# Kernel tuning notes

Measured on AMD Instinct MI355X. Metric: run time of the kernel, lower is better.

The kernel has to match this reference:

```python
import jax, jax.numpy as jnp
import numpy as np

NUM_HEADS = 16
ROPE_THETA = 10000.0


def apply_rope(x, pos):
    # x: [b, h, s, d_head]; rotates consecutive pairs (2i, 2i+1)
    d = x.shape[-1]
    inv_freq = ROPE_THETA ** (-jnp.arange(0, d, 2, dtype=x.dtype) / d)  # [d/2]
    ang = pos.astype(x.dtype)[:, None] * inv_freq[None, :]              # [s, d/2]
    cos, sin = jnp.cos(ang), jnp.sin(ang)
    x1, x2 = x[..., 0::2], x[..., 1::2]
    rot = jnp.stack([x1 * cos - x2 * sin, x1 * sin + x2 * cos], axis=-1)
    return rot.reshape(x.shape)


def setup_inputs() -> dict:
    key = jax.random.key(0)
    k1, k2, k3 = jax.random.split(key, 3)
    d_model = 1024
    x = jax.random.normal(k1, (4, 2048, d_model), dtype=jnp.float32)
    wqkv = jax.random.normal(k2, (3 * d_model, d_model), dtype=jnp.float32) * 0.02
    wout = jax.random.normal(k3, (d_model, d_model), dtype=jnp.float32) * 0.02
    return {"x": x, "wqkv": wqkv, "wout": wout}


def reference(x, wqkv, wout):
    b, s, d_model = x.shape
    h = NUM_HEADS
    d_head = d_model // h

    qkv = jnp.einsum("bsd,ed->bse", x, wqkv)              # [b, s, 3*d_model]
    q, k, v = jnp.split(qkv, 3, axis=-1)

    def split_heads(t):  # [b, s, d_model] -> [b, h, s, d_head]
        return t.reshape(b, s, h, d_head).transpose(0, 2, 1, 3)

    q, k, v = split_heads(q), split_heads(k), split_heads(v)

    pos = jnp.arange(s)
    q = apply_rope(q, pos)
    k = apply_rope(k, pos)

    scale = 1.0 / jnp.sqrt(jnp.asarray(d_head, dtype=x.dtype))
    scores = jnp.einsum("bhqd,bhkd->bhqk", q, k) * scale   # [b, h, s, s]
    causal = jnp.tril(jnp.ones((s, s), dtype=bool))
    scores = jnp.where(causal, scores, jnp.finfo(scores.dtype).min)
    attn = jax.nn.softmax(scores, axis=-1)
    y = jnp.einsum("bhqk,bhkd->bhqd", attn, v)             # [b, h, s, d_head]
    y = y.transpose(0, 2, 1, 3).reshape(b, s, d_model)
    return jnp.einsum("bsd,ed->bse", y, wout)
```

## Files before the change

### kernel.cpp

```cpp
#include <hip/hip_runtime.h>
#include <stdint.h>

typedef uint16_t u16;
typedef __bf16 bf16x8 __attribute__((ext_vector_type(8)));
typedef float   f32x4 __attribute__((ext_vector_type(4)));
typedef uint16_t u16x2 __attribute__((ext_vector_type(2)));
typedef uint16_t u16x4 __attribute__((ext_vector_type(4)));
typedef uint16_t u16x8 __attribute__((ext_vector_type(8)));
typedef float   f32x4g __attribute__((ext_vector_type(4)));

#define DEV __device__ __forceinline__

DEV u16 f2bf(float f) {
  __bf16 h = (__bf16)f;
  return __builtin_bit_cast(u16, h);
}
DEV float bf2f(u16 u) {
  union { uint32_t u; float f; } v; v.u = ((uint32_t)u) << 16;
  return v.f;
}
DEV float exp2fast(float x) {
  float r; asm("v_exp_f32 %0, %1" : "=v"(r) : "v"(x)); return r;
}

DEV void gload_lds16(const u16* g, u16* l) {
  __builtin_amdgcn_global_load_lds((const __attribute__((address_space(1))) void*)g,
                                   (__attribute__((address_space(3))) void*)l,
                                   16, 0, 0);
}

__global__ void sctab_kernel(float2* __restrict__ tab) {
  const int idx = blockIdx.x * 256 + threadIdx.x;
  const int s = idx >> 5, i = idx & 31;
  const float invf = (float)exp2(-2.0 * (double)i / 64.0 * 13.287712379549449);
  float sn, cs;
  sincosf((float)s * invf, &sn, &cs);
  tab[idx] = make_float2(cs, sn);
}

__global__ void cvt3_kernel(const float* __restrict__ a, u16* __restrict__ da,
                            const float* __restrict__ b, u16* __restrict__ db,
                            const float* __restrict__ c, u16* __restrict__ dc) {
  int i = blockIdx.x * 256 + threadIdx.x;
  const float* s; u16* d; int off;
  if (i < 2097152)      { s = a; d = da; off = i; }
  else if (i < 2883584) { s = b; d = db; off = i - 2097152; }
  else                  { s = c; d = dc; off = i - 2883584; }
  f32x4g v = ((const f32x4g*)s)[off];
  u16 tmp[4] = {f2bf(v[0]), f2bf(v[1]), f2bf(v[2]), f2bf(v[3])};
  *(uint64_t*)(d + (size_t)off * 4) = *(const uint64_t*)tmp;
}

__global__ __launch_bounds__(256) void gemm_qkv(const u16* __restrict__ A,
                                                const u16* __restrict__ B,
                                                const float2* __restrict__ tab,
                                                u16* __restrict__ Qh,
                                                u16* __restrict__ Kh,
                                                u16* __restrict__ Vt) {
  constexpr int K = 1024;
  constexpr int BK = 32;
  __shared__ __align__(16) u16 SM[4][128 * BK];
  const int t = threadIdx.x;
  const int w = t >> 6, l = t & 63;
  const int l4 = l >> 4, l15 = l & 15;

  const int nbx = gridDim.x;
  const int nwg = gridDim.x * gridDim.y;
  const int orig = blockIdx.y * nbx + blockIdx.x;
  const int wgid = (orig & 7) * (nwg >> 3) + (orig >> 3);
  const int bm = (wgid / nbx) * 128, bn = (wgid % nbx) * 128;

  const int wr = (w >> 1) * 64, wc = (w & 1) * 64;

  const int srow = w * 32 + (l >> 2);
  const int scol = (l & 3) * 8;
  const u16* gA = A + (size_t)(bm + srow) * K + scol;
  const u16* gB = B + (size_t)(bn + srow) * K + scol;

  f32x4 acc[4][4];
#pragma unroll
  for (int m = 0; m < 4; ++m)
#pragma unroll
    for (int n = 0; n < 4; ++n) acc[m][n] = f32x4{0.f, 0.f, 0.f, 0.f};

  const int nkt = K / BK;

  auto stage = [&](int kt, int buf) {
    const u16* a0 = gA + (size_t)kt * BK;
    const u16* b0 = gB + (size_t)kt * BK;
    gload_lds16(a0,                  &SM[buf][(w * 32) * BK]);
    gload_lds16(a0 + (size_t)16 * K, &SM[buf][(w * 32 + 16) * BK]);
    gload_lds16(b0,                  &SM[2 + buf][(w * 32) * BK]);
    gload_lds16(b0 + (size_t)16 * K, &SM[2 + buf][(w * 32 + 16) * BK]);
  };

  stage(0, 0);
  __syncthreads();
  for (int kt = 0; kt < nkt; ++kt) {
    const int buf = kt & 1;
    if (kt + 1 < nkt) stage(kt + 1, buf ^ 1);
    bf16x8 af[4], bfr[4];
#pragma unroll
    for (int m = 0; m < 4; ++m) af[m]  = *(const bf16x8*)&SM[buf][(wr + m * 16 + l15) * BK + l4 * 8];
#pragma unroll
    for (int n = 0; n < 4; ++n) bfr[n] = *(const bf16x8*)&SM[2 + buf][(wc + n * 16 + l15) * BK + l4 * 8];
#pragma unroll
    for (int m = 0; m < 4; ++m)
#pragma unroll
      for (int n = 0; n < 4; ++n)
        acc[m][n] = __builtin_amdgcn_mfma_f32_16x16x32_bf16(af[m], bfr[n], acc[m][n], 0, 0, 0);
    __syncthreads();
  }

  constexpr int LDW = 132;
  float* Lf = (float*)SM;
  const int part = bn >> 10;
  const int cb = bn & 1023;
  const float qs = (part == 0) ? 0.18033688011112042f : 1.0f;
  u16* const Out = (part == 0) ? Qh : Kh;
  const int lrbase = (w >> 1) * 16 + l4 * 4;
  const int lcbase = (w & 1) * 64 + l15;

#pragma unroll
  for (int m = 0; m < 4; ++m) {
    if (m) __syncthreads();
#pragma unroll
    for (int n = 0; n < 4; ++n)
#pragma unroll
      for (int r = 0; r < 4; ++r)
        Lf[(lrbase + r) * LDW + lcbase + n * 16] = acc[m][n][r];
    __syncthreads();

    if (part != 2) {
      const int rr = t >> 3;
      const int c0 = (t & 7) * 16;
      const int grow = bm + (rr >> 4) * 64 + m * 16 + (rr & 15);
      const int bb = grow >> 11, ss = grow & 2047;
      float f[16];
#pragma unroll
      for (int j = 0; j < 4; ++j)
        *(f32x4g*)&f[j * 4] = *(const f32x4g*)&Lf[rr * LDW + c0 + j * 4];
      const int cc0 = cb + c0;
      const int hh = cc0 >> 6, dd0 = cc0 & 63;
      const float2* tp = &tab[(size_t)ss * 32 + (dd0 >> 1)];
      u16 ob[16];
#pragma unroll
      for (int jp = 0; jp < 8; ++jp) {
        const float2 cs2 = tp[jp];
        ob[2 * jp]     = f2bf((f[2 * jp] * cs2.x - f[2 * jp + 1] * cs2.y) * qs);
        ob[2 * jp + 1] = f2bf((f[2 * jp] * cs2.y + f[2 * jp + 1] * cs2.x) * qs);
      }
      u16* op = Out + ((size_t)(bb * 16 + hh) * 2048 + ss) * 64 + dd0;
      *(u16x8*)op       = *(u16x8*)ob;
      *(u16x8*)(op + 8) = *(u16x8*)(ob + 8);
    } else {
      const int c = t >> 1, half = t & 1;
      const int cc = cb + c, hh = cc >> 6, dd = cc & 63;
      const int g0 = bm + half * 64 + m * 16;
      const int bb = g0 >> 11, ss0 = g0 & 2047;
      u16 ob[16];
#pragma unroll
      for (int j = 0; j < 16; ++j)
        ob[j] = f2bf(Lf[(half * 16 + j) * LDW + c]);
      u16* vp = Vt + ((size_t)(bb * 16 + hh) * 64 + dd) * 2048 + ss0;
      *(u16x8*)vp       = *(u16x8*)ob;
      *(u16x8*)(vp + 8) = *(u16x8*)(ob + 8);
    }
  }
}

template<bool OUT_BF16>
__global__ __launch_bounds__(256) void gemm_bt(const u16* __restrict__ A,
                                               const u16* __restrict__ B,
                                               void* __restrict__ Cv,
                                               int M, int N, int K) {
  constexpr int BK = 32;
  __shared__ __align__(16) u16 As[2][128 * BK];
  __shared__ __align__(16) u16 Bs[2][128 * BK];
  const int t = threadIdx.x;
  const int w = t >> 6, l = t & 63;
  const int l4 = l >> 4, l15 = l & 15;

  const int nbx = gridDim.x;
  const int nwg = gridDim.x * gridDim.y;
  const int orig = blockIdx.y * nbx + blockIdx.x;
  const int wgid = (orig & 7) * (nwg >> 3) + (orig >> 3);
  const int bm = (wgid / nbx) * 128, bn = (wgid % nbx) * 128;

  const int wr = (w >> 1) * 64, wc = (w & 1) * 64;

  const int srow = w * 32 + (l >> 2);
  const int scol = (l & 3) * 8;
  const u16* gA = A + (size_t)(bm + srow) * K + scol;
  const u16* gB = B + (size_t)(bn + srow) * K + scol;

  f32x4 acc[4][4];
#pragma unroll
  for (int m = 0; m < 4; ++m)
#pragma unroll
    for (int n = 0; n < 4; ++n) acc[m][n] = f32x4{0.f, 0.f, 0.f, 0.f};

  const int nkt = K / BK;

  auto stage = [&](int kt, int buf) {
    const u16* a0 = gA + (size_t)kt * BK;
    const u16* b0 = gB + (size_t)kt * BK;
    gload_lds16(a0,                  &As[buf][(w * 32) * BK]);
    gload_lds16(a0 + (size_t)16 * K, &As[buf][(w * 32 + 16) * BK]);
    gload_lds16(b0,                  &Bs[buf][(w * 32) * BK]);
    gload_lds16(b0 + (size_t)16 * K, &Bs[buf][(w * 32 + 16) * BK]);
  };

  stage(0, 0);
  __syncthreads();
  for (int kt = 0; kt < nkt; ++kt) {
    const int buf = kt & 1;
    if (kt + 1 < nkt) stage(kt + 1, buf ^ 1);
    bf16x8 af[4], bfr[4];
#pragma unroll
    for (int m = 0; m < 4; ++m) af[m]  = *(const bf16x8*)&As[buf][(wr + m * 16 + l15) * BK + l4 * 8];
#pragma unroll
    for (int n = 0; n < 4; ++n) bfr[n] = *(const bf16x8*)&Bs[buf][(wc + n * 16 + l15) * BK + l4 * 8];
#pragma unroll
    for (int m = 0; m < 4; ++m)
#pragma unroll
      for (int n = 0; n < 4; ++n)
        acc[m][n] = __builtin_amdgcn_mfma_f32_16x16x32_bf16(af[m], bfr[n], acc[m][n], 0, 0, 0);
    __syncthreads();
  }

#pragma unroll
  for (int m = 0; m < 4; ++m) {
    const int row0 = bm + wr + m * 16 + l4 * 4;
#pragma unroll
    for (int n = 0; n < 4; ++n) {
      const int col = bn + wc + n * 16 + l15;
#pragma unroll
      for (int r = 0; r < 4; ++r) {
        if (OUT_BF16) ((u16*)Cv)[(size_t)(row0 + r) * N + col] = f2bf(acc[m][n][r]);
        else          ((float*)Cv)[(size_t)(row0 + r) * N + col] = acc[m][n][r];
      }
    }
  }
}

__global__ __launch_bounds__(256, 5) void attn_kernel(const u16* __restrict__ Qh,
                                                      const u16* __restrict__ Kh,
                                                      const u16* __restrict__ Vt,
                                                      u16* __restrict__ Y) {
  __shared__ __align__(16) u16 Ks[64][72];
  __shared__ __align__(16) u16 Vs[64][72];
  __shared__ __align__(16) u16 Ps[4][16][72];
  const int t = threadIdx.x, w = t >> 6, l = t & 63;
  const int l4 = l >> 4, l15 = l & 15;
  const int bid = blockIdx.x;
  const int s   = 31 - (bid >> 6);
  const int bh  = bid & 63;
  const int b = bh >> 4, h = bh & 15;
  const int q0 = s * 64 + w * 16;
  const u16* Qb = Qh + (size_t)bh * 2048 * 64;
  const u16* Kb = Kh + (size_t)bh * 2048 * 64;
  const u16* Vb = Vt + (size_t)bh * 64 * 2048;

  bf16x8 qf[2];
#pragma unroll
  for (int ks = 0; ks < 2; ++ks)
    qf[ks] = *(const bf16x8*)(Qb + (size_t)(q0 + l15) * 64 + ks * 32 + l4 * 8);

  f32x4 o[4];
#pragma unroll
  for (int nd = 0; nd < 4; ++nd) o[nd] = f32x4{0.f, 0.f, 0.f, 0.f};
  float lsum = 0.f;

  const int sr = t >> 3;
  const int scol = (t & 7) * 8;
  const int nkv = s + 1;

  u16x8 rk0 = *(const u16x8*)(Kb + (size_t)sr * 64 + scol);
  u16x8 rk1 = *(const u16x8*)(Kb + (size_t)(sr + 32) * 64 + scol);
  u16x8 rv0 = *(const u16x8*)(Vb + (size_t)sr * 2048 + scol);
  u16x8 rv1 = *(const u16x8*)(Vb + (size_t)(sr + 32) * 2048 + scol);

  for (int kv = 0; kv < nkv; ++kv) {
    const int kv0 = kv * 64;
    __syncthreads();
    *(u16x8*)&Ks[sr][scol]      = rk0;
    *(u16x8*)&Ks[sr + 32][scol] = rk1;
    *(u16x8*)&Vs[sr][scol]      = rv0;
    *(u16x8*)&Vs[sr + 32][scol] = rv1;
    __syncthreads();
    if (kv + 1 < nkv) {
      const int n0 = kv0 + 64;
      rk0 = *(const u16x8*)(Kb + (size_t)(n0 + sr) * 64 + scol);
      rk1 = *(const u16x8*)(Kb + (size_t)(n0 + sr + 32) * 64 + scol);
      rv0 = *(const u16x8*)(Vb + (size_t)sr * 2048 + n0 + scol);
      rv1 = *(const u16x8*)(Vb + (size_t)(sr + 32) * 2048 + n0 + scol);
    }

    f32x4 sfr[4];
    __builtin_amdgcn_s_setprio(1);
#pragma unroll
    for (int n = 0; n < 4; ++n) {
      bf16x8 kf0 = *(const bf16x8*)&Ks[n * 16 + l15][l4 * 8];
      bf16x8 kf1 = *(const bf16x8*)&Ks[n * 16 + l15][32 + l4 * 8];
      f32x4 a = f32x4{0.f, 0.f, 0.f, 0.f};
      a = __builtin_amdgcn_mfma_f32_16x16x32_bf16(kf0, qf[0], a, 0, 0, 0);
      a = __builtin_amdgcn_mfma_f32_16x16x32_bf16(kf1, qf[1], a, 0, 0, 0);
      sfr[n] = a;
    }
    __builtin_amdgcn_s_setprio(0);
    if (kv == s) {
      const int q = q0 + l15;
#pragma unroll
      for (int n = 0; n < 4; ++n)
#pragma unroll
        for (int r = 0; r < 4; ++r)
          if (kv0 + n * 16 + l4 * 4 + r > q) sfr[n][r] = -1e30f;
    }
    float rs = 0.f;
#pragma unroll
    for (int n = 0; n < 4; ++n) {
#pragma unroll
      for (int r = 0; r < 4; ++r) {
        const float pv = exp2fast(sfr[n][r]);
        sfr[n][r] = pv; rs += pv;
      }
      u16x4 pk = {f2bf(sfr[n][0]), f2bf(sfr[n][1]), f2bf(sfr[n][2]), f2bf(sfr[n][3])};
      *(u16x4*)&Ps[w][l15][n * 16 + l4 * 4] = pk;
    }
    lsum += rs;

    bf16x8 vfr[4][2];
#pragma unroll
    for (int nd = 0; nd < 4; ++nd) {
      vfr[nd][0] = *(const bf16x8*)&Vs[nd * 16 + l15][l4 * 8];
      vfr[nd][1] = *(const bf16x8*)&Vs[nd * 16 + l15][32 + l4 * 8];
    }
    bf16x8 pf0 = *(const bf16x8*)&Ps[w][l15][l4 * 8];
    bf16x8 pf1 = *(const bf16x8*)&Ps[w][l15][32 + l4 * 8];
    __builtin_amdgcn_s_setprio(1);
#pragma unroll
    for (int nd = 0; nd < 4; ++nd) {
      o[nd] = __builtin_amdgcn_mfma_f32_16x16x32_bf16(pf0, vfr[nd][0], o[nd], 0, 0, 0);
      o[nd] = __builtin_amdgcn_mfma_f32_16x16x32_bf16(pf1, vfr[nd][1], o[nd], 0, 0, 0);
    }
    __builtin_amdgcn_s_setprio(0);
  }

  lsum += __shfl_xor(lsum, 16);
  lsum += __shfl_xor(lsum, 32);
  const float li = 1.0f / lsum;
  float lb[4];
#pragma unroll
  for (int r = 0; r < 4; ++r) lb[r] = __shfl(li, (l & 48) | (l4 * 4 + r));
#pragma unroll
  for (int r = 0; r < 4; ++r) {
    const size_t row = (size_t)b * 2048 + q0 + l4 * 4 + r;
#pragma unroll
    for (int nd = 0; nd < 4; ++nd)
      Y[row * 1024 + h * 64 + nd * 16 + l15] = f2bf(o[nd][r] * lb[r]);
  }
}

extern "C" void kernel_launch(void* const* d_in, const int* in_sizes, int n_in,
                              void* d_out, int out_size, void* d_ws, size_t ws_size,
                              hipStream_t stream) {
  const float* x    = (const float*)d_in[0];
  const float* wqkv = (const float*)d_in[1];
  const float* wout = (const float*)d_in[2];
  float* out = (float*)d_out;
  char* ws = (char*)d_ws;

  u16* x_bf    = (u16*)(ws);
  u16* Y       = x_bf;
  u16* wqkv_bf = (u16*)(ws + 16777216);
  u16* wout_bf = (u16*)(ws + 23068672);
  float2* tab  = (float2*)(ws + 25165824);
  u16* Qh      = (u16*)(ws + 75497472);
  u16* Kh      = (u16*)(ws + 92274688);
  u16* Vt      = (u16*)(ws + 109051904);

  sctab_kernel<<<256, 256, 0, stream>>>(tab);
  cvt3_kernel<<<12288, 256, 0, stream>>>(x, x_bf, wqkv, wqkv_bf, wout, wout_bf);
  gemm_qkv<<<dim3(24, 64), 256, 0, stream>>>(x_bf, wqkv_bf, tab, Qh, Kh, Vt);
  attn_kernel<<<2048, 256, 0, stream>>>(Qh, Kh, Vt, Y);
  gemm_bt<false><<<dim3(8, 64), 256, 0, stream>>>(Y, wout_bf, out, 8192, 1024, 1024);
}
```

Measured before the change: 204.7 us.

## Double query rows per attention block to reuse K/V tiles across two query fragments

Each attention block now covers 128 query rows, with every wave handling two 16-row fragments, so every K/V tile staged in shared memory feeds twice as many MFMAs and global K/V traffic is halved. The grid shrinks to 1024 blocks, and block-to-sequence-tile mapping is changed to interleave long and short causal tiles for load balance. In exchange it uses more registers and LDS, drops the occupancy hint from launch bounds, and does some wasted masked work on the diagonal tiles.

```diff
diff --git a/kernel.cpp b/kernel.cpp
--- a/kernel.cpp
+++ b/kernel.cpp
@@ -244,37 +244,46 @@
   }
 }
 
-__global__ __launch_bounds__(256, 5) void attn_kernel(const u16* __restrict__ Qh,
-                                                      const u16* __restrict__ Kh,
-                                                      const u16* __restrict__ Vt,
-                                                      u16* __restrict__ Y) {
+__global__ __launch_bounds__(256) void attn_kernel(const u16* __restrict__ Qh,
+                                                   const u16* __restrict__ Kh,
+                                                   const u16* __restrict__ Vt,
+                                                   u16* __restrict__ Y) {
   __shared__ __align__(16) u16 Ks[64][72];
   __shared__ __align__(16) u16 Vs[64][72];
-  __shared__ __align__(16) u16 Ps[4][16][72];
+  __shared__ __align__(16) u16 Ps[4][32][72];
   const int t = threadIdx.x, w = t >> 6, l = t & 63;
   const int l4 = l >> 4, l15 = l & 15;
   const int bid = blockIdx.x;
-  const int s   = 31 - (bid >> 6);
-  const int bh  = bid & 63;
+  const int sidx = (bid + (bid >> 8)) & 15;
+  const int s = (sidx & 1) ? (sidx >> 1) : (15 - (sidx >> 1));
+  const int bh = bid >> 4;
   const int b = bh >> 4, h = bh & 15;
-  const int q0 = s * 64 + w * 16;
+  const int qb0 = s * 128 + w * 32;
+  const int qb1 = qb0 + 16;
   const u16* Qb = Qh + (size_t)bh * 2048 * 64;
   const u16* Kb = Kh + (size_t)bh * 2048 * 64;
   const u16* Vb = Vt + (size_t)bh * 64 * 2048;
 
-  bf16x8 qf[2];
-#pragma unroll
-  for (int ks = 0; ks < 2; ++ks)
-    qf[ks] = *(const bf16x8*)(Qb + (size_t)(q0 + l15) * 64 + ks * 32 + l4 * 8);
-
-  f32x4 o[4];
-#pragma unroll
-  for (int nd = 0; nd < 4; ++nd) o[nd] = f32x4{0.f, 0.f, 0.f, 0.f};
-  float lsum = 0.f;
+  bf16x8 qf[2][2];
+  {
+    const int qb[2] = {qb0, qb1};
+#pragma unroll
+    for (int m = 0; m < 2; ++m)
+#pragma unroll
+      for (int ks = 0; ks < 2; ++ks)
+        qf[m][ks] = *(const bf16x8*)(Qb + (size_t)(qb[m] + l15) * 64 + ks * 32 + l4 * 8);
+  }
+
+  f32x4 o[2][4];
+#pragma unroll
+  for (int m = 0; m < 2; ++m)
+#pragma unroll
+    for (int nd = 0; nd < 4; ++nd) o[m][nd] = f32x4{0.f, 0.f, 0.f, 0.f};
+  float lsum[2] = {0.f, 0.f};
 
   const int sr = t >> 3;
   const int scol = (t & 7) * 8;
-  const int nkv = s + 1;
+  const int nkv = 2 * s + 2;
 
   u16x8 rk0 = *(const u16x8*)(Kb + (size_t)sr * 64 + scol);
   u16x8 rk1 = *(const u16x8*)(Kb + (size_t)(sr + 32) * 64 + scol);
@@ -297,38 +306,43 @@
       rv1 = *(const u16x8*)(Vb + (size_t)(sr + 32) * 2048 + n0 + scol);
     }
 
-    f32x4 sfr[4];
-    __builtin_amdgcn_s_setprio(1);
-#pragma unroll
-    for (int n = 0; n < 4; ++n) {
-      bf16x8 kf0 = *(const bf16x8*)&Ks[n * 16 + l15][l4 * 8];
-      bf16x8 kf1 = *(const bf16x8*)&Ks[n * 16 + l15][32 + l4 * 8];
-      f32x4 a = f32x4{0.f, 0.f, 0.f, 0.f};
-      a = __builtin_amdgcn_mfma_f32_16x16x32_bf16(kf0, qf[0], a, 0, 0, 0);
-      a = __builtin_amdgcn_mfma_f32_16x16x32_bf16(kf1, qf[1], a, 0, 0, 0);
-      sfr[n] = a;
-    }
-    __builtin_amdgcn_s_setprio(0);
-    if (kv == s) {
-      const int q = q0 + l15;
-#pragma unroll
-      for (int n = 0; n < 4; ++n)
-#pragma unroll
-        for (int r = 0; r < 4; ++r)
-          if (kv0 + n * 16 + l4 * 4 + r > q) sfr[n][r] = -1e30f;
-    }
-    float rs = 0.f;
-#pragma unroll
-    for (int n = 0; n < 4; ++n) {
-#pragma unroll
-      for (int r = 0; r < 4; ++r) {
-        const float pv = exp2fast(sfr[n][r]);
-        sfr[n][r] = pv; rs += pv;
-      }
-      u16x4 pk = {f2bf(sfr[n][0]), f2bf(sfr[n][1]), f2bf(sfr[n][2]), f2bf(sfr[n][3])};
-      *(u16x4*)&Ps[w][l15][n * 16 + l4 * 4] = pk;
-    }
-    lsum += rs;
+    auto SCORE = [&](int m, int qbm) {
+      f32x4 sfr[4];
+      __builtin_amdgcn_s_setprio(1);
+#pragma unroll
+      for (int n = 0; n < 4; ++n) {
+        bf16x8 kf0 = *(const bf16x8*)&Ks[n * 16 + l15][l4 * 8];
+        bf16x8 kf1 = *(const bf16x8*)&Ks[n * 16 + l15][32 + l4 * 8];
+        f32x4 a = f32x4{0.f, 0.f, 0.f, 0.f};
+        a = __builtin_amdgcn_mfma_f32_16x16x32_bf16(kf0, qf[m][0], a, 0, 0, 0);
+        a = __builtin_amdgcn_mfma_f32_16x16x32_bf16(kf1, qf[m][1], a, 0, 0, 0);
+        sfr[n] = a;
+      }
+      __builtin_amdgcn_s_setprio(0);
+      if (kv0 + 63 > qbm) {
+        const int q = qbm + l15;
+#pragma unroll
+        for (int n = 0; n < 4; ++n)
+#pragma unroll
+          for (int r = 0; r < 4; ++r)
+            if (kv0 + n * 16 + l4 * 4 + r > q) sfr[n][r] = -1e30f;
+      }
+      float rs = 0.f;
+#pragma unroll
+      for (int n = 0; n < 4; ++n) {
+#pragma unroll
+        for (int r = 0; r < 4; ++r) {
+          const float pv = exp2fast(sfr[n][r]);
+          sfr[n][r] = pv; rs += pv;
+        }
+        u16x4 pk = {f2bf(sfr[n][0]), f2bf(sfr[n][1]), f2bf(sfr[n][2]), f2bf(sfr[n][3])};
+        *(u16x4*)&Ps[w][m * 16 + l15][n * 16 + l4 * 4] = pk;
+      }
+      lsum[m] += rs;
+    };
+
+    SCORE(1, qb1);
+    SCORE(0, qb0);
 
     bf16x8 vfr[4][2];
 #pragma unroll
@@ -336,29 +350,38 @@
       vfr[nd][0] = *(const bf16x8*)&Vs[nd * 16 + l15][l4 * 8];
       vfr[nd][1] = *(const bf16x8*)&Vs[nd * 16 + l15][32 + l4 * 8];
     }
-    bf16x8 pf0 = *(const bf16x8*)&Ps[w][l15][l4 * 8];
-    bf16x8 pf1 = *(const bf16x8*)&Ps[w][l15][32 + l4 * 8];
-    __builtin_amdgcn_s_setprio(1);
-#pragma unroll
-    for (int nd = 0; nd < 4; ++nd) {
-      o[nd] = __builtin_amdgcn_mfma_f32_16x16x32_bf16(pf0, vfr[nd][0], o[nd], 0, 0, 0);
-      o[nd] = __builtin_amdgcn_mfma_f32_16x16x32_bf16(pf1, vfr[nd][1], o[nd], 0, 0, 0);
+
+    auto PV = [&](int m) {
+      bf16x8 pf0 = *(const bf16x8*)&Ps[w][m * 16 + l15][l4 * 8];
+      bf16x8 pf1 = *(const bf16x8*)&Ps[w][m * 16 + l15][32 + l4 * 8];
+      __builtin_amdgcn_s_setprio(1);
+#pragma unroll
+      for (int nd = 0; nd < 4; ++nd) {
+        o[m][nd] = __builtin_amdgcn_mfma_f32_16x16x32_bf16(pf0, vfr[nd][0], o[m][nd], 0, 0, 0);
+        o[m][nd] = __builtin_amdgcn_mfma_f32_16x16x32_bf16(pf1, vfr[nd][1], o[m][nd], 0, 0, 0);
+      }
+      __builtin_amdgcn_s_setprio(0);
+    };
+    PV(1);
+    PV(0);
+  }
+
+  const int qb[2] = {qb0, qb1};
+#pragma unroll
+  for (int m = 0; m < 2; ++m) {
+    lsum[m] += __shfl_xor(lsum[m], 16);
+    lsum[m] += __shfl_xor(lsum[m], 32);
+    const float li = 1.0f / lsum[m];
+    float lb[4];
+#pragma unroll
+    for (int r = 0; r < 4; ++r) lb[r] = __shfl(li, (l & 48) | (l4 * 4 + r));
+#pragma unroll
+    for (int r = 0; r < 4; ++r) {
+      const size_t row = (size_t)b * 2048 + qb[m] + l4 * 4 + r;
+#pragma unroll
+      for (int nd = 0; nd < 4; ++nd)
+        Y[row * 1024 + h * 64 + nd * 16 + l15] = f2bf(o[m][nd][r] * lb[r]);
     }
-    __builtin_amdgcn_s_setprio(0);
-  }
-
-  lsum += __shfl_xor(lsum, 16);
-  lsum += __shfl_xor(lsum, 32);
-  const float li = 1.0f / lsum;
-  float lb[4];
-#pragma unroll
-  for (int r = 0; r < 4; ++r) lb[r] = __shfl(li, (l & 48) | (l4 * 4 + r));
-#pragma unroll
-  for (int r = 0; r < 4; ++r) {
-    const size_t row = (size_t)b * 2048 + q0 + l4 * 4 + r;
-#pragma unroll
-    for (int nd = 0; nd < 4; ++nd)
-      Y[row * 1024 + h * 64 + nd * 16 + l15] = f2bf(o[nd][r] * lb[r]);
   }
 }
 
@@ -383,6 +406,6 @@
   sctab_kernel<<<256, 256, 0, stream>>>(tab);
   cvt3_kernel<<<12288, 256, 0, stream>>>(x, x_bf, wqkv, wqkv_bf, wout, wout_bf);
   gemm_qkv<<<dim3(24, 64), 256, 0, stream>>>(x_bf, wqkv_bf, tab, Qh, Kh, Vt);
-  attn_kernel<<<2048, 256, 0, stream>>>(Qh, Kh, Vt, Y);
+  attn_kernel<<<1024, 256, 0, stream>>>(Qh, Kh, Vt, Y);
   gemm_bt<false><<<dim3(8, 64), 256, 0, stream>>>(Y, wout_bf, out, 8192, 1024, 1024);
 }
```

New measurement: 210.1 us. +2.6%, slower.
